# Performance work log

Hardware: AMD Instinct MI355X
Metric: run time of the kernel (lower is better)

## Reference

```python
import jax, jax.numpy as jnp
import numpy as np

N_NODES = 50000
N_EDGES = 800000
IN_C, HID_C, OUT_C = 128, 128, 64


def setup_inputs() -> dict:
    key = jax.random.key(0)
    ks = jax.random.split(key, 8)
    x = jax.random.normal(ks[0], (N_NODES, IN_C), dtype=jnp.float32)
    edge_index = jax.random.randint(ks[1], (2, N_EDGES), 0, N_NODES, dtype=jnp.int32)
    edge_weight = jax.random.uniform(ks[2], (N_EDGES,), dtype=jnp.float32)
    node_type = jax.random.randint(ks[3], (N_NODES,), 0, 4, dtype=jnp.int32)
    s1 = 1.0 / np.sqrt(IN_C)
    s2 = 1.0 / np.sqrt(HID_C)
    return {
        "x": x,
        "edge_index": edge_index,
        "edge_weight": edge_weight,
        "node_type": node_type,
        "W_l1": jax.random.normal(ks[4], (HID_C, IN_C), dtype=jnp.float32) * s1,
        "b_l1": jnp.zeros((HID_C,), dtype=jnp.float32),
        "W_r1": jax.random.normal(ks[5], (HID_C, IN_C), dtype=jnp.float32) * s1,
        "W_l2": jax.random.normal(ks[6], (OUT_C, HID_C), dtype=jnp.float32) * s2,
        "b_l2": jnp.zeros((OUT_C,), dtype=jnp.float32),
        "W_r2": jax.random.normal(ks[7], (OUT_C, HID_C), dtype=jnp.float32) * s2,
    }


def _sage_conv(h, src, dst, edge_weight, W_l, b_l, W_r, num_nodes):
    # message: edge_weight * x_src, mean-aggregated at dst (PyG SAGEConv mean aggr)
    msg = h[src] * edge_weight[:, None]                                  # [E, C]
    agg = jax.ops.segment_sum(msg, dst, num_segments=num_nodes)          # [N, C]
    deg = jax.ops.segment_sum(jnp.ones_like(edge_weight), dst, num_segments=num_nodes)
    agg = agg / jnp.maximum(deg, 1.0)[:, None]
    # out = lin_l(agg) + lin_r(root); bias only on lin_l (PyG convention)
    return agg @ W_l.T + b_l + h @ W_r.T


def reference(x, edge_index, edge_weight, node_type, W_l1, b_l1, W_r1, W_l2, b_l2, W_r2):
    num_nodes = x.shape[0]
    src, dst = edge_index[0], edge_index[1]
    h = _sage_conv(x, src, dst, edge_weight, W_l1, b_l1, W_r1, num_nodes)
    h = jax.nn.relu(h)  # dropout p=0.0 -> identity
    out = _sage_conv(h, src, dst, edge_weight, W_l2, b_l2, W_r2, num_nodes)
    return out
```

## Files before the change

kernel.cpp:

```cpp
#include <hip/hip_runtime.h>

constexpr int IN_C  = 128;
constexpr int HID_C = 128;
constexpr int OUT_C = 64;

constexpr int BSHIFT    = 6;
constexpr int BNODES    = 64;
constexpr int NBUCK_MAX = 1024;
constexpr int CAP       = 2048;
constexpr int EPB       = 4096;

constexpr float W10_DEC = 1.0f / 1023.0f;

typedef short bf16x8 __attribute__((ext_vector_type(8)));
typedef float f32x4  __attribute__((ext_vector_type(4)));
typedef float f32x2  __attribute__((ext_vector_type(2)));

__device__ __forceinline__ unsigned short f2b(float f) {
    unsigned u = __float_as_uint(f);
    unsigned r = (u + 0x7fffu + ((u >> 16) & 1u)) >> 16;
    return (unsigned short)r;
}
__device__ __forceinline__ float b2f_lo(unsigned u) { return __uint_as_float(u << 16); }
__device__ __forceinline__ float b2f_hi(unsigned u) { return __uint_as_float(u & 0xffff0000u); }
__device__ __forceinline__ unsigned char f2fp8(float f) {
    int p = __builtin_amdgcn_cvt_pk_fp8_f32(f, f, 0, false);
    return (unsigned char)(p & 0xff);
}
__device__ __forceinline__ float wdec(unsigned rec) {
    return (float)(rec >> 16) * W10_DEC;
}

struct Acc8 {
    float a0 = 0, a1 = 0, a2 = 0, a3 = 0, a4 = 0, a5 = 0, a6 = 0, a7 = 0;
    __device__ __forceinline__ void acc_fp8(uint2 v, float wt) {
        f32x2 p0 = __builtin_amdgcn_cvt_pk_f32_fp8(v.x, false);
        f32x2 p1 = __builtin_amdgcn_cvt_pk_f32_fp8(v.x, true);
        f32x2 p2 = __builtin_amdgcn_cvt_pk_f32_fp8(v.y, false);
        f32x2 p3 = __builtin_amdgcn_cvt_pk_f32_fp8(v.y, true);
        a0 = fmaf(p0[0], wt, a0); a1 = fmaf(p0[1], wt, a1);
        a2 = fmaf(p1[0], wt, a2); a3 = fmaf(p1[1], wt, a3);
        a4 = fmaf(p2[0], wt, a4); a5 = fmaf(p2[1], wt, a5);
        a6 = fmaf(p3[0], wt, a6); a7 = fmaf(p3[1], wt, a7);
    }
    __device__ __forceinline__ void acc_bf16(uint4 v, float wt) {
        a0 = fmaf(b2f_lo(v.x), wt, a0); a1 = fmaf(b2f_hi(v.x), wt, a1);
        a2 = fmaf(b2f_lo(v.y), wt, a2); a3 = fmaf(b2f_hi(v.y), wt, a3);
        a4 = fmaf(b2f_lo(v.z), wt, a4); a5 = fmaf(b2f_hi(v.z), wt, a5);
        a6 = fmaf(b2f_lo(v.w), wt, a6); a7 = fmaf(b2f_hi(v.w), wt, a7);
    }
};


__global__ __launch_bounds__(256) void k_init(
    int* __restrict__ bcnt, int NBUCK,
    const float* __restrict__ wa, const float* __restrict__ wb,
    const float* __restrict__ wc, const float* __restrict__ wd,
    unsigned short* __restrict__ wab, unsigned short* __restrict__ wbb,
    unsigned short* __restrict__ wcb, unsigned short* __restrict__ wdb) {
    if (blockIdx.x == 0) {
        for (int i = threadIdx.x; i < NBUCK; i += 256) bcnt[i] = 0;
        return;
    }
    const int NW1 = HID_C * IN_C, NW3 = OUT_C * HID_C;
    int off = ((blockIdx.x - 1) * 256 + threadIdx.x) * 4;
    if (off >= 2 * NW1 + 2 * NW3) return;
    const float* s; unsigned short* d;
    if (off < NW1) { s = wa; d = wab; }
    else { off -= NW1;
        if (off < NW1) { s = wb; d = wbb; }
        else { off -= NW1;
            if (off < NW3) { s = wc; d = wcb; }
            else { off -= NW3; s = wd; d = wdb; }
        }
    }
    float4 v = *reinterpret_cast<const float4*>(s + off);
    ushort4 o;
    o.x = f2b(v.x); o.y = f2b(v.y); o.z = f2b(v.z); o.w = f2b(v.w);
    *reinterpret_cast<ushort4*>(d + off) = o;
}


__device__ __forceinline__ void gemm1_body(
    int bx, const float* __restrict__ A, const unsigned short* __restrict__ Wm,
    const unsigned short* __restrict__ Wr, unsigned char* __restrict__ Om,
    unsigned short* __restrict__ Or, int N) {
    constexpr int K = IN_C;
    int wave = threadIdx.x >> 6;
    int lane = threadIdx.x & 63;
    int tile = bx * 4 + wave;
    int m0 = tile * 16;
    if (m0 >= N) return;
    int lm = lane & 15;
    int quad = lane >> 4;
    int row = min(m0 + lm, N - 1);

    bf16x8 afrag[K / 32];
#pragma unroll
    for (int kk = 0; kk < K / 32; kk++) {
        const float* ap = A + (size_t)row * K + kk * 32 + quad * 8;
        float4 u0 = *reinterpret_cast<const float4*>(ap);
        float4 u1 = *reinterpret_cast<const float4*>(ap + 4);
        bf16x8 a;
        a[0] = (short)f2b(u0.x); a[1] = (short)f2b(u0.y);
        a[2] = (short)f2b(u0.z); a[3] = (short)f2b(u0.w);
        a[4] = (short)f2b(u1.x); a[5] = (short)f2b(u1.y);
        a[6] = (short)f2b(u1.z); a[7] = (short)f2b(u1.w);
        afrag[kk] = a;
    }
#pragma unroll
    for (int j = 0; j < HID_C / 16; j++) {
        const unsigned short* wrow = Wm + (size_t)(j * 16 + lm) * K + quad * 8;
        f32x4 acc = {0.f, 0.f, 0.f, 0.f};
#pragma unroll
        for (int kk = 0; kk < K / 32; kk++) {
            bf16x8 b = *reinterpret_cast<const bf16x8*>(wrow + kk * 32);
            acc = __builtin_amdgcn_mfma_f32_16x16x32_bf16(afrag[kk], b, acc, 0, 0, 0);
        }
#pragma unroll
        for (int r = 0; r < 4; r++) {
            int node = m0 + quad * 4 + r;
            if (node < N) Om[(size_t)node * HID_C + j * 16 + lm] = f2fp8(acc[r]);
        }
    }
#pragma unroll
    for (int j = 0; j < HID_C / 16; j++) {
        const unsigned short* wrow = Wr + (size_t)(j * 16 + lm) * K + quad * 8;
        f32x4 acc = {0.f, 0.f, 0.f, 0.f};
#pragma unroll
        for (int kk = 0; kk < K / 32; kk++) {
            bf16x8 b = *reinterpret_cast<const bf16x8*>(wrow + kk * 32);
            acc = __builtin_amdgcn_mfma_f32_16x16x32_bf16(afrag[kk], b, acc, 0, 0, 0);
        }
#pragma unroll
        for (int r = 0; r < 4; r++) {
            int node = m0 + quad * 4 + r;
            if (node < N) Or[(size_t)node * HID_C + j * 16 + lm] = f2b(acc[r]);
        }
    }
}


__global__ __launch_bounds__(256) void k_fill_gemm1(
    const int* __restrict__ src, const int* __restrict__ dst,
    const float* __restrict__ ew, int E, int NBUCK, int EBLK,
    int* __restrict__ bcnt, unsigned int* __restrict__ brec,
    const float* __restrict__ x, const unsigned short* __restrict__ wl1b,
    const unsigned short* __restrict__ wr1b, unsigned char* __restrict__ msg1,
    unsigned short* __restrict__ root1, int N) {
    if (blockIdx.x >= EBLK) {
        gemm1_body(blockIdx.x - EBLK, x, wl1b, wr1b, msg1, root1, N);
        return;
    }
    __shared__ int lh[NBUCK_MAX], lbase[NBUCK_MAX], lcnt[NBUCK_MAX];
    for (int i = threadIdx.x; i < NBUCK; i += 256) { lh[i] = 0; lcnt[i] = 0; }
    __syncthreads();
    int base = blockIdx.x * EPB;
    unsigned int rec[EPB / 256];
    int bkt[EPB / 256];
#pragma unroll
    for (int i = 0; i < EPB / 256; i++) {
        int e = base + i * 256 + threadIdx.x;
        if (e < E) {
            int d = dst[e];
            int b = d >> BSHIFT;
            unsigned w10 = (unsigned)(ew[e] * 1023.0f + 0.5f);
            rec[i] = (unsigned)(src[e] & 0xffff) | ((unsigned)(d & (BNODES - 1)) << 16)
                   | (w10 << 22);
            bkt[i] = b;
            atomicAdd(&lh[b], 1);
        } else {
            bkt[i] = -1;
        }
    }
    __syncthreads();
    for (int i = threadIdx.x; i < NBUCK; i += 256) {
        int v = lh[i];
        lbase[i] = v ? (i * CAP + atomicAdd(&bcnt[i], v)) : 0;
    }
    __syncthreads();
#pragma unroll
    for (int i = 0; i < EPB / 256; i++) {
        if (bkt[i] >= 0) {
            int loc = atomicAdd(&lcnt[bkt[i]], 1);
            brec[(size_t)lbase[bkt[i]] + loc] = rec[i];
        }
    }
}


constexpr int HSTRIDE = HID_C + 8;

__global__ __launch_bounds__(256) void k_csr_comb_gemm2(
    const unsigned int* __restrict__ brec, const int* __restrict__ bcnt, int N,
    int2* __restrict__ row_range, unsigned int* __restrict__ csr,
    const unsigned char* __restrict__ msg1,
    const unsigned short* __restrict__ root1,
    const float* __restrict__ b1,
    const unsigned short* __restrict__ wl2b,
    const unsigned short* __restrict__ wr2b,
    unsigned short* __restrict__ msg2,
    unsigned short* __restrict__ root2) {
    __shared__ int lh[BNODES], lex[BNODES], lsc[BNODES], lcnt[BNODES];
    __shared__ unsigned int lcsr[CAP];
    __shared__ unsigned short hls[BNODES * HSTRIDE];
    int b = blockIdx.x, t = threadIdx.x;
    if (t < BNODES) { lh[t] = 0; lcnt[t] = 0; }
    __syncthreads();
    int beg = b * CAP;
    int cnt = bcnt[b];
    for (int e = t; e < cnt; e += 256)
        atomicAdd(&lh[(brec[beg + e] >> 16) & (BNODES - 1)], 1);
    __syncthreads();
    if (t < BNODES) lsc[t] = lh[t];
    __syncthreads();
    for (int d = 1; d < BNODES; d <<= 1) {
        int v = (t >= d && t < BNODES) ? lsc[t - d] : 0;
        __syncthreads();
        if (t < BNODES) lsc[t] += v;
        __syncthreads();
    }
    if (t < BNODES) lex[t] = lsc[t] - lh[t];
    __syncthreads();
    int node_base = b << BSHIFT;
    if (t < BNODES && node_base + t < N)
        row_range[node_base + t] = make_int2(beg + lex[t], beg + lsc[t]);
    for (int e = t; e < cnt; e += 256) {
        unsigned int r = brec[beg + e];
        int d = (r >> 16) & (BNODES - 1);
        int loc = atomicAdd(&lcnt[d], 1);
        lcsr[lex[d] + loc] = (r & 0xffff) | ((r >> 22) << 16);
    }
    __syncthreads();
    for (int e = t; e < cnt; e += 256) csr[beg + e] = lcsr[e];
    int c8 = (t & 15) * 8;
#pragma unroll
    for (int g = 0; g < BNODES / 16; g++) {
        int nl = g * 16 + (t >> 4);
        int node = node_base + nl;
        bool valid = node < N;
        int eb = lex[nl], ee = lsc[nl];
        Acc8 ac;
        int e = eb;
        for (; e + 3 < ee; e += 4) {
            unsigned int r0e = lcsr[e],     r1e = lcsr[e + 1];
            unsigned int r2e = lcsr[e + 2], r3e = lcsr[e + 3];
            uint2 v0 = *reinterpret_cast<const uint2*>(msg1 + (size_t)(r0e & 0xffff) * HID_C + c8);
            uint2 v1 = *reinterpret_cast<const uint2*>(msg1 + (size_t)(r1e & 0xffff) * HID_C + c8);
            uint2 v2 = *reinterpret_cast<const uint2*>(msg1 + (size_t)(r2e & 0xffff) * HID_C + c8);
            uint2 v3 = *reinterpret_cast<const uint2*>(msg1 + (size_t)(r3e & 0xffff) * HID_C + c8);
            ac.acc_fp8(v0, wdec(r0e)); ac.acc_fp8(v1, wdec(r1e));
            ac.acc_fp8(v2, wdec(r2e)); ac.acc_fp8(v3, wdec(r3e));
        }
        for (; e < ee; e++) {
            unsigned int r0e = lcsr[e];
            uint2 v0 = *reinterpret_cast<const uint2*>(msg1 + (size_t)(r0e & 0xffff) * HID_C + c8);
            ac.acc_fp8(v0, wdec(r0e));
        }
        uint4 pk = {0, 0, 0, 0};
        if (valid) {
            float inv = 1.0f / fmaxf((float)(ee - eb), 1.0f);
            uint4 rv = *reinterpret_cast<const uint4*>(root1 + (size_t)node * HID_C + c8);
            float4 b0 = *reinterpret_cast<const float4*>(b1 + c8);
            float4 b1v = *reinterpret_cast<const float4*>(b1 + c8 + 4);
            float o0 = fmaxf(fmaf(ac.a0, inv, b0.x + b2f_lo(rv.x)), 0.f);
            float o1 = fmaxf(fmaf(ac.a1, inv, b0.y + b2f_hi(rv.x)), 0.f);
            float o2 = fmaxf(fmaf(ac.a2, inv, b0.z + b2f_lo(rv.y)), 0.f);
            float o3 = fmaxf(fmaf(ac.a3, inv, b0.w + b2f_hi(rv.y)), 0.f);
            float o4 = fmaxf(fmaf(ac.a4, inv, b1v.x + b2f_lo(rv.z)), 0.f);
            float o5 = fmaxf(fmaf(ac.a5, inv, b1v.y + b2f_hi(rv.z)), 0.f);
            float o6 = fmaxf(fmaf(ac.a6, inv, b1v.z + b2f_lo(rv.w)), 0.f);
            float o7 = fmaxf(fmaf(ac.a7, inv, b1v.w + b2f_hi(rv.w)), 0.f);
            pk.x = (unsigned)f2b(o0) | ((unsigned)f2b(o1) << 16);
            pk.y = (unsigned)f2b(o2) | ((unsigned)f2b(o3) << 16);
            pk.z = (unsigned)f2b(o4) | ((unsigned)f2b(o5) << 16);
            pk.w = (unsigned)f2b(o6) | ((unsigned)f2b(o7) << 16);
        }
        *reinterpret_cast<uint4*>(&hls[nl * HSTRIDE + c8]) = pk;
    }
    __syncthreads();
    int wave = t >> 6;
    int lane = t & 63;
    int lm = lane & 15;
    int quad = lane >> 4;
#pragma unroll
    for (int mt = 0; mt < BNODES / 16; mt++) {
        int m0 = node_base + mt * 16;
        bf16x8 afrag[4];
#pragma unroll
        for (int kk = 0; kk < 4; kk++)
            afrag[kk] = *reinterpret_cast<const bf16x8*>(
                &hls[(mt * 16 + lm) * HSTRIDE + kk * 32 + quad * 8]);
#pragma unroll
        for (int t2 = 0; t2 < 2; t2++) {
            int jt = wave * 2 + t2;
            const unsigned short* W = (jt < 4) ? wl2b : wr2b;
            unsigned short* O = (jt < 4) ? msg2 : root2;
            int j = jt & 3;
            const unsigned short* wrow = W + (size_t)(j * 16 + lm) * HID_C + quad * 8;
            f32x4 acc = {0.f, 0.f, 0.f, 0.f};
#pragma unroll
            for (int kk = 0; kk < 4; kk++) {
                bf16x8 bb = *reinterpret_cast<const bf16x8*>(wrow + kk * 32);
                acc = __builtin_amdgcn_mfma_f32_16x16x32_bf16(afrag[kk], bb, acc, 0, 0, 0);
            }
#pragma unroll
            for (int r = 0; r < 4; r++) {
                int nd = m0 + quad * 4 + r;
                if (nd < N) O[(size_t)nd * OUT_C + j * 16 + lm] = f2b(acc[r]);
            }
        }
    }
}


__global__ __launch_bounds__(256) void k_combine2(
    const unsigned short* __restrict__ msg2,
    const unsigned short* __restrict__ root2,
    const float* __restrict__ bias,
    const int2* __restrict__ row_range, const unsigned int* __restrict__ crec,
    float* __restrict__ out, int N) {
    constexpr int C = OUT_C;
    constexpr int LPN = C / 8;
    constexpr int NPB = 256 / LPN;
    int tid = threadIdx.x;
    int node = blockIdx.x * NPB + tid / LPN;
    if (node >= N) return;
    int c8 = (tid % LPN) * 8;
    int2 rr = row_range[node];
    int beg = rr.x, end = rr.y;

    Acc8 ac;
    int e = beg;
    for (; e + 3 < end; e += 4) {
        unsigned int r0e = crec[e],     r1e = crec[e + 1];
        unsigned int r2e = crec[e + 2], r3e = crec[e + 3];
        uint4 v0 = *reinterpret_cast<const uint4*>(msg2 + (size_t)(r0e & 0xffff) * C + c8);
        uint4 v1 = *reinterpret_cast<const uint4*>(msg2 + (size_t)(r1e & 0xffff) * C + c8);
        uint4 v2 = *reinterpret_cast<const uint4*>(msg2 + (size_t)(r2e & 0xffff) * C + c8);
        uint4 v3 = *reinterpret_cast<const uint4*>(msg2 + (size_t)(r3e & 0xffff) * C + c8);
        ac.acc_bf16(v0, wdec(r0e)); ac.acc_bf16(v1, wdec(r1e));
        ac.acc_bf16(v2, wdec(r2e)); ac.acc_bf16(v3, wdec(r3e));
    }
    for (; e < end; e++) {
        unsigned int r0e = crec[e];
        uint4 v0 = *reinterpret_cast<const uint4*>(msg2 + (size_t)(r0e & 0xffff) * C + c8);
        ac.acc_bf16(v0, wdec(r0e));
    }
    float inv = 1.0f / fmaxf((float)(end - beg), 1.0f);
    uint4 rv = *reinterpret_cast<const uint4*>(root2 + (size_t)node * C + c8);
    float4 b0 = *reinterpret_cast<const float4*>(bias + c8);
    float4 b1 = *reinterpret_cast<const float4*>(bias + c8 + 4);
    float* op = out + (size_t)node * C + c8;
    *reinterpret_cast<float4*>(op) = make_float4(
        fmaf(ac.a0, inv, b0.x + b2f_lo(rv.x)), fmaf(ac.a1, inv, b0.y + b2f_hi(rv.x)),
        fmaf(ac.a2, inv, b0.z + b2f_lo(rv.y)), fmaf(ac.a3, inv, b0.w + b2f_hi(rv.y)));
    *reinterpret_cast<float4*>(op + 4) = make_float4(
        fmaf(ac.a4, inv, b1.x + b2f_lo(rv.z)), fmaf(ac.a5, inv, b1.y + b2f_hi(rv.z)),
        fmaf(ac.a6, inv, b1.z + b2f_lo(rv.w)), fmaf(ac.a7, inv, b1.w + b2f_hi(rv.w)));
}


extern "C" void kernel_launch(void* const* d_in, const int* in_sizes, int n_in,
                              void* d_out, int out_size, void* d_ws, size_t ws_size,
                              hipStream_t stream) {
    const float* x    = (const float*)d_in[0];
    const int*   eidx = (const int*)d_in[1];
    const float* ew   = (const float*)d_in[2];
    const float* W_l1 = (const float*)d_in[4];
    const float* b_l1 = (const float*)d_in[5];
    const float* W_r1 = (const float*)d_in[6];
    const float* W_l2 = (const float*)d_in[7];
    const float* b_l2 = (const float*)d_in[8];
    const float* W_r2 = (const float*)d_in[9];
    float* out = (float*)d_out;

    const int N = in_sizes[0] / IN_C;
    const int E = in_sizes[1] / 2;
    const int* src = eidx;
    const int* dst = eidx + E;
    const int NBUCK = (N + BNODES - 1) >> BSHIFT;
    const int EBLK = (E + EPB - 1) / EPB;
    const int WBLK = ((2 * HID_C * IN_C + 2 * OUT_C * HID_C) / 4 + 255) / 256;

    char* p = (char*)d_ws;
    auto carve = [&](size_t bytes) -> char* {
        char* r = p;
        p += (bytes + 255) & ~(size_t)255;
        return r;
    };
    int*  bcnt      = (int*)carve((size_t)NBUCK * 4);
    int2* row_range = (int2*)carve((size_t)N * 8);
    unsigned int* brec = (unsigned int*)carve((size_t)NBUCK * CAP * 4);
    unsigned int* csr  = (unsigned int*)carve((size_t)NBUCK * CAP * 4);
    unsigned short* wl1b = (unsigned short*)carve((size_t)HID_C * IN_C * 2);
    unsigned short* wr1b = (unsigned short*)carve((size_t)HID_C * IN_C * 2);
    unsigned short* wl2b = (unsigned short*)carve((size_t)OUT_C * HID_C * 2);
    unsigned short* wr2b = (unsigned short*)carve((size_t)OUT_C * HID_C * 2);
    unsigned char*  msg1 = (unsigned char*)carve((size_t)N * HID_C);
    unsigned short* root1 = (unsigned short*)carve((size_t)N * HID_C * 2);
    unsigned short* msg2 = (unsigned short*)carve((size_t)N * OUT_C * 2);
    unsigned short* root2 = (unsigned short*)carve((size_t)N * OUT_C * 2);

    int tiles = (N + 15) / 16;
    int gblk = (tiles + 3) / 4;

    k_init<<<1 + WBLK, 256, 0, stream>>>(bcnt, NBUCK,
        W_l1, W_r1, W_l2, W_r2, wl1b, wr1b, wl2b, wr2b);
    k_fill_gemm1<<<EBLK + gblk, 256, 0, stream>>>(
        src, dst, ew, E, NBUCK, EBLK, bcnt, brec,
        x, wl1b, wr1b, msg1, root1, N);
    k_csr_comb_gemm2<<<NBUCK, 256, 0, stream>>>(
        brec, bcnt, N, row_range, csr, msg1, root1, b_l1,
        wl2b, wr2b, msg2, root2);
    k_combine2<<<(N + 31) / 32, 256, 0, stream>>>(
        msg2, root2, b_l2, row_range, csr, out, N);
}
```

Measured before the change: 173.4 us.

## Drop weight-conversion kernel; convert fp32 weights to bf16 inline in GEMMs

Removes the k_init kernel that pre-converted the four weight matrices to bf16. The GEMM bodies now load fp32 weights and round them to bf16 in registers at each use, and the bucket counters are cleared with hipMemsetAsync. The aim is to save one kernel launch and its dependency, at the cost of twice the weight bytes read from cache and extra conversion ALU work inside every GEMM tile. The final combine kernel also gains an 8-edge unrolled gather loop to keep more loads in flight.

```diff
diff --git a/kernel.cpp b/kernel.cpp
--- a/kernel.cpp
+++ b/kernel.cpp
@@ -29,6 +29,16 @@
 }
 __device__ __forceinline__ float wdec(unsigned rec) {
     return (float)(rec >> 16) * W10_DEC;
+}
+__device__ __forceinline__ bf16x8 ldw8(const float* wp) {
+    float4 u0 = *reinterpret_cast<const float4*>(wp);
+    float4 u1 = *reinterpret_cast<const float4*>(wp + 4);
+    bf16x8 a;
+    a[0] = (short)f2b(u0.x); a[1] = (short)f2b(u0.y);
+    a[2] = (short)f2b(u0.z); a[3] = (short)f2b(u0.w);
+    a[4] = (short)f2b(u1.x); a[5] = (short)f2b(u1.y);
+    a[6] = (short)f2b(u1.z); a[7] = (short)f2b(u1.w);
+    return a;
 }
 
 struct Acc8 {
@@ -52,38 +62,9 @@
 };
 
 
-__global__ __launch_bounds__(256) void k_init(
-    int* __restrict__ bcnt, int NBUCK,
-    const float* __restrict__ wa, const float* __restrict__ wb,
-    const float* __restrict__ wc, const float* __restrict__ wd,
-    unsigned short* __restrict__ wab, unsigned short* __restrict__ wbb,
-    unsigned short* __restrict__ wcb, unsigned short* __restrict__ wdb) {
-    if (blockIdx.x == 0) {
-        for (int i = threadIdx.x; i < NBUCK; i += 256) bcnt[i] = 0;
-        return;
-    }
-    const int NW1 = HID_C * IN_C, NW3 = OUT_C * HID_C;
-    int off = ((blockIdx.x - 1) * 256 + threadIdx.x) * 4;
-    if (off >= 2 * NW1 + 2 * NW3) return;
-    const float* s; unsigned short* d;
-    if (off < NW1) { s = wa; d = wab; }
-    else { off -= NW1;
-        if (off < NW1) { s = wb; d = wbb; }
-        else { off -= NW1;
-            if (off < NW3) { s = wc; d = wcb; }
-            else { off -= NW3; s = wd; d = wdb; }
-        }
-    }
-    float4 v = *reinterpret_cast<const float4*>(s + off);
-    ushort4 o;
-    o.x = f2b(v.x); o.y = f2b(v.y); o.z = f2b(v.z); o.w = f2b(v.w);
-    *reinterpret_cast<ushort4*>(d + off) = o;
-}
-
-
 __device__ __forceinline__ void gemm1_body(
-    int bx, const float* __restrict__ A, const unsigned short* __restrict__ Wm,
-    const unsigned short* __restrict__ Wr, unsigned char* __restrict__ Om,
+    int bx, const float* __restrict__ A, const float* __restrict__ Wm,
+    const float* __restrict__ Wr, unsigned char* __restrict__ Om,
     unsigned short* __restrict__ Or, int N) {
     constexpr int K = IN_C;
     int wave = threadIdx.x >> 6;
@@ -97,24 +78,16 @@
 
     bf16x8 afrag[K / 32];
 #pragma unroll
-    for (int kk = 0; kk < K / 32; kk++) {
-        const float* ap = A + (size_t)row * K + kk * 32 + quad * 8;
-        float4 u0 = *reinterpret_cast<const float4*>(ap);
-        float4 u1 = *reinterpret_cast<const float4*>(ap + 4);
-        bf16x8 a;
-        a[0] = (short)f2b(u0.x); a[1] = (short)f2b(u0.y);
-        a[2] = (short)f2b(u0.z); a[3] = (short)f2b(u0.w);
-        a[4] = (short)f2b(u1.x); a[5] = (short)f2b(u1.y);
-        a[6] = (short)f2b(u1.z); a[7] = (short)f2b(u1.w);
-        afrag[kk] = a;
-    }
+    for (int kk = 0; kk < K / 32; kk++)
+        afrag[kk] = ldw8(A + (size_t)row * K + kk * 32 + quad * 8);
+
 #pragma unroll
     for (int j = 0; j < HID_C / 16; j++) {
-        const unsigned short* wrow = Wm + (size_t)(j * 16 + lm) * K + quad * 8;
+        const float* wrow = Wm + (size_t)(j * 16 + lm) * K + quad * 8;
         f32x4 acc = {0.f, 0.f, 0.f, 0.f};
 #pragma unroll
         for (int kk = 0; kk < K / 32; kk++) {
-            bf16x8 b = *reinterpret_cast<const bf16x8*>(wrow + kk * 32);
+            bf16x8 b = ldw8(wrow + kk * 32);
             acc = __builtin_amdgcn_mfma_f32_16x16x32_bf16(afrag[kk], b, acc, 0, 0, 0);
         }
 #pragma unroll
@@ -125,11 +98,11 @@
     }
 #pragma unroll
     for (int j = 0; j < HID_C / 16; j++) {
-        const unsigned short* wrow = Wr + (size_t)(j * 16 + lm) * K + quad * 8;
+        const float* wrow = Wr + (size_t)(j * 16 + lm) * K + quad * 8;
         f32x4 acc = {0.f, 0.f, 0.f, 0.f};
 #pragma unroll
         for (int kk = 0; kk < K / 32; kk++) {
-            bf16x8 b = *reinterpret_cast<const bf16x8*>(wrow + kk * 32);
+            bf16x8 b = ldw8(wrow + kk * 32);
             acc = __builtin_amdgcn_mfma_f32_16x16x32_bf16(afrag[kk], b, acc, 0, 0, 0);
         }
 #pragma unroll
@@ -145,11 +118,11 @@
     const int* __restrict__ src, const int* __restrict__ dst,
     const float* __restrict__ ew, int E, int NBUCK, int EBLK,
     int* __restrict__ bcnt, unsigned int* __restrict__ brec,
-    const float* __restrict__ x, const unsigned short* __restrict__ wl1b,
-    const unsigned short* __restrict__ wr1b, unsigned char* __restrict__ msg1,
+    const float* __restrict__ x, const float* __restrict__ W_l1,
+    const float* __restrict__ W_r1, unsigned char* __restrict__ msg1,
     unsigned short* __restrict__ root1, int N) {
     if (blockIdx.x >= EBLK) {
-        gemm1_body(blockIdx.x - EBLK, x, wl1b, wr1b, msg1, root1, N);
+        gemm1_body(blockIdx.x - EBLK, x, W_l1, W_r1, msg1, root1, N);
         return;
     }
     __shared__ int lh[NBUCK_MAX], lbase[NBUCK_MAX], lcnt[NBUCK_MAX];
@@ -197,8 +170,8 @@
     const unsigned char* __restrict__ msg1,
     const unsigned short* __restrict__ root1,
     const float* __restrict__ b1,
-    const unsigned short* __restrict__ wl2b,
-    const unsigned short* __restrict__ wr2b,
+    const float* __restrict__ W_l2,
+    const float* __restrict__ W_r2,
     unsigned short* __restrict__ msg2,
     unsigned short* __restrict__ root2) {
     __shared__ int lh[BNODES], lex[BNODES], lsc[BNODES], lcnt[BNODES];
@@ -294,14 +267,14 @@
 #pragma unroll
         for (int t2 = 0; t2 < 2; t2++) {
             int jt = wave * 2 + t2;
-            const unsigned short* W = (jt < 4) ? wl2b : wr2b;
+            const float* W = (jt < 4) ? W_l2 : W_r2;
             unsigned short* O = (jt < 4) ? msg2 : root2;
             int j = jt & 3;
-            const unsigned short* wrow = W + (size_t)(j * 16 + lm) * HID_C + quad * 8;
+            const float* wrow = W + (size_t)(j * 16 + lm) * HID_C + quad * 8;
             f32x4 acc = {0.f, 0.f, 0.f, 0.f};
 #pragma unroll
             for (int kk = 0; kk < 4; kk++) {
-                bf16x8 bb = *reinterpret_cast<const bf16x8*>(wrow + kk * 32);
+                bf16x8 bb = ldw8(wrow + kk * 32);
                 acc = __builtin_amdgcn_mfma_f32_16x16x32_bf16(afrag[kk], bb, acc, 0, 0, 0);
             }
 #pragma unroll
@@ -332,6 +305,24 @@
 
     Acc8 ac;
     int e = beg;
+    for (; e + 7 < end; e += 8) {
+        unsigned int r0e = crec[e],     r1e = crec[e + 1];
+        unsigned int r2e = crec[e + 2], r3e = crec[e + 3];
+        unsigned int r4e = crec[e + 4], r5e = crec[e + 5];
+        unsigned int r6e = crec[e + 6], r7e = crec[e + 7];
+        uint4 v0 = *reinterpret_cast<const uint4*>(msg2 + (size_t)(r0e & 0xffff) * C + c8);
+        uint4 v1 = *reinterpret_cast<const uint4*>(msg2 + (size_t)(r1e & 0xffff) * C + c8);
+        uint4 v2 = *reinterpret_cast<const uint4*>(msg2 + (size_t)(r2e & 0xffff) * C + c8);
+        uint4 v3 = *reinterpret_cast<const uint4*>(msg2 + (size_t)(r3e & 0xffff) * C + c8);
+        uint4 v4 = *reinterpret_cast<const uint4*>(msg2 + (size_t)(r4e & 0xffff) * C + c8);
+        uint4 v5 = *reinterpret_cast<const uint4*>(msg2 + (size_t)(r5e & 0xffff) * C + c8);
+        uint4 v6 = *reinterpret_cast<const uint4*>(msg2 + (size_t)(r6e & 0xffff) * C + c8);
+        uint4 v7 = *reinterpret_cast<const uint4*>(msg2 + (size_t)(r7e & 0xffff) * C + c8);
+        ac.acc_bf16(v0, wdec(r0e)); ac.acc_bf16(v1, wdec(r1e));
+        ac.acc_bf16(v2, wdec(r2e)); ac.acc_bf16(v3, wdec(r3e));
+        ac.acc_bf16(v4, wdec(r4e)); ac.acc_bf16(v5, wdec(r5e));
+        ac.acc_bf16(v6, wdec(r6e)); ac.acc_bf16(v7, wdec(r7e));
+    }
     for (; e + 3 < end; e += 4) {
         unsigned int r0e = crec[e],     r1e = crec[e + 1];
         unsigned int r2e = crec[e + 2], r3e = crec[e + 3];
@@ -381,7 +372,6 @@
     const int* dst = eidx + E;
     const int NBUCK = (N + BNODES - 1) >> BSHIFT;
     const int EBLK = (E + EPB - 1) / EPB;
-    const int WBLK = ((2 * HID_C * IN_C + 2 * OUT_C * HID_C) / 4 + 255) / 256;
 
     char* p = (char*)d_ws;
     auto carve = [&](size_t bytes) -> char* {
@@ -393,10 +383,6 @@
     int2* row_range = (int2*)carve((size_t)N * 8);
     unsigned int* brec = (unsigned int*)carve((size_t)NBUCK * CAP * 4);
     unsigned int* csr  = (unsigned int*)carve((size_t)NBUCK * CAP * 4);
-    unsigned short* wl1b = (unsigned short*)carve((size_t)HID_C * IN_C * 2);
-    unsigned short* wr1b = (unsigned short*)carve((size_t)HID_C * IN_C * 2);
-    unsigned short* wl2b = (unsigned short*)carve((size_t)OUT_C * HID_C * 2);
-    unsigned short* wr2b = (unsigned short*)carve((size_t)OUT_C * HID_C * 2);
     unsigned char*  msg1 = (unsigned char*)carve((size_t)N * HID_C);
     unsigned short* root1 = (unsigned short*)carve((size_t)N * HID_C * 2);
     unsigned short* msg2 = (unsigned short*)carve((size_t)N * OUT_C * 2);
@@ -405,14 +391,13 @@
     int tiles = (N + 15) / 16;
     int gblk = (tiles + 3) / 4;
 
-    k_init<<<1 + WBLK, 256, 0, stream>>>(bcnt, NBUCK,
-        W_l1, W_r1, W_l2, W_r2, wl1b, wr1b, wl2b, wr2b);
+    hipMemsetAsync(bcnt, 0, (size_t)NBUCK * 4, stream);
     k_fill_gemm1<<<EBLK + gblk, 256, 0, stream>>>(
         src, dst, ew, E, NBUCK, EBLK, bcnt, brec,
-        x, wl1b, wr1b, msg1, root1, N);
+        x, W_l1, W_r1, msg1, root1, N);
     k_csr_comb_gemm2<<<NBUCK, 256, 0, stream>>>(
         brec, bcnt, N, row_range, csr, msg1, root1, b_l1,
-        wl2b, wr2b, msg2, root2);
+        W_l2, W_r2, msg2, root2);
     k_combine2<<<(N + 31) / 32, 256, 0, stream>>>(
         msg2, root2, b_l2, row_range, csr, out, N);
 }
```

Measured after the change: 204.9 us. 18.2% more time.
